# Optimization experiments

Measured on AMD Instinct MI355X. Metric: run time of the kernel, lower is better.

## Reference

```python
import jax, jax.numpy as jnp
import numpy as np

TOTAL_WORDS = 10000
EMB = 100
SEQ = 80
UNITS = 64


def setup_inputs() -> dict:
    key = jax.random.key(0)
    ks = jax.random.split(key, 10)
    B = 16384
    tokens = jax.random.randint(ks[0], (B, SEQ), 0, TOTAL_WORDS, dtype=jnp.int32)
    s = 0.05
    emb = jax.random.normal(ks[1], (TOTAL_WORDS, EMB), jnp.float32) * s
    Wx0 = jax.random.normal(ks[2], (EMB, UNITS), jnp.float32) * s
    Wh0 = jax.random.normal(ks[3], (UNITS, UNITS), jnp.float32) * s
    b0 = jnp.zeros((UNITS,), jnp.float32)
    Wx1 = jax.random.normal(ks[4], (UNITS, UNITS), jnp.float32) * s
    Wh1 = jax.random.normal(ks[5], (UNITS, UNITS), jnp.float32) * s
    b1 = jnp.zeros((UNITS,), jnp.float32)
    Wout = jax.random.normal(ks[6], (UNITS, 1), jnp.float32) * s
    bout = jnp.zeros((1,), jnp.float32)
    return {"tokens": tokens, "emb": emb, "Wx0": Wx0, "Wh0": Wh0, "b0": b0,
            "Wx1": Wx1, "Wh1": Wh1, "b1": b1, "Wout": Wout, "bout": bout}


def reference(tokens, emb, Wx0, Wh0, b0, Wx1, Wh1, b1, Wout, bout):
    # Embedding lookup: [B, SEQ, EMB]
    x = emb[tokens]
    B = tokens.shape[0]
    # time-major for scan: [SEQ, B, EMB]
    xt = jnp.transpose(x, (1, 0, 2))
    h0 = jnp.zeros((B, UNITS), x.dtype)
    h1 = jnp.zeros((B, UNITS), x.dtype)

    def step(carry, x_t):
        h0, h1 = carry
        # SimpleRNNCell (inference, dropout inactive): h' = tanh(x Wx + h Wh + b)
        h0n = jnp.tanh(x_t @ Wx0 + h0 @ Wh0 + b0)
        h1n = jnp.tanh(h0n @ Wx1 + h1 @ Wh1 + b1)
        return (h0n, h1n), None

    (h0, h1), _ = jax.lax.scan(step, (h0, h1), xt)
    logits = h1 @ Wout + bout  # [B, 1]
    return jax.nn.sigmoid(logits)
```

## Files before the change

kernel.cpp:

```cpp
#include <hip/hip_runtime.h>

#define TOTAL_WORDS 10000
#define EMB 100
#define SEQ 80
#define UNITS 64
#define BATCH 16384


typedef _Float16 f16x8 __attribute__((ext_vector_type(8)));
typedef _Float16 h2    __attribute__((ext_vector_type(2)));
typedef __fp16   fp16x2r __attribute__((ext_vector_type(2)));
typedef float    f32x4 __attribute__((ext_vector_type(4)));
typedef unsigned int u32;
typedef u32      u32x4 __attribute__((ext_vector_type(4)));

__device__ __forceinline__ u32 tanh_pk(float x, float y) {
    h2 v = __builtin_bit_cast(h2, __builtin_amdgcn_cvt_pkrtz(x, y));
    const _Float16 c3 = (_Float16)(-0.33333333f);
    const _Float16 c5 = (_Float16)(0.13333333f);
    h2 x2 = v * v;
    h2 p  = x2 * c5 + c3;
    h2 x3 = x2 * v;
    h2 r  = x3 * p + v;
    return __builtin_bit_cast(u32, r);
}

__device__ __forceinline__ f16x8 tanh_frag(f32x4 a, f32x4 b) {
    u32x4 w;
    w.x = tanh_pk(a[0], a[1]);
    w.y = tanh_pk(a[2], a[3]);
    w.z = tanh_pk(b[0], b[1]);
    w.w = tanh_pk(b[2], b[3]);
    return __builtin_bit_cast(f16x8, w);
}

__global__ void prep_kernel(const float* __restrict__ emb,
                            const float* __restrict__ Wx0,
                            const float* __restrict__ b0,
                            const float* __restrict__ Wh0,
                            const float* __restrict__ Wx1,
                            const float* __restrict__ Wh1,
                            float* __restrict__ embW,
                            _Float16* __restrict__ wfrags) {
    int b = blockIdx.x;
    if (b < 250) {
        __shared__ float wx[EMB * UNITS];
        for (int i = threadIdx.x; i < EMB * UNITS; i += 256)
            wx[i] = Wx0[i];
        __syncthreads();
        const int u = threadIdx.x & 63;
        const int wvi = threadIdx.x >> 6;
        const int vbase = b * 40 + wvi * 10;
        const float bias = b0[u];
        float acc[10];
#pragma unroll
        for (int i = 0; i < 10; ++i) acc[i] = bias;
        const float* er = emb + vbase * EMB;
#pragma unroll 4
        for (int k = 0; k < EMB; ++k) {
            float wxv = wx[k * UNITS + u];
#pragma unroll
            for (int i = 0; i < 10; ++i)
                acc[i] = fmaf(er[i * EMB + k], wxv, acc[i]);
        }
#pragma unroll
        for (int i = 0; i < 10; ++i)
            embW[(vbase + i) * UNITS + u] = acc[i];
    } else {
        int e = (b - 250) * 256 + threadIdx.x;
        int mat = e >> 12;
        int ee = e & 4095;
        int f = ee >> 9;
        int mt = f >> 1, kf = f & 1;
        int rr = ee & 511;
        int l = rr >> 3, j = rr & 7;
        int k = kf * 32 + (l >> 4) * 8 + j;
        int mm = l & 15;
        int col = 32 * (mt >> 1) + 8 * (mm >> 2) + 4 * (mt & 1) + (mm & 3);
        const float* W = (mat == 0) ? Wh0 : (mat == 1) ? Wx1 : Wh1;
        wfrags[e] = (_Float16)W[k * UNITS + col];
    }
}

#define MF(A, B, C) __builtin_amdgcn_mfma_f32_16x16x32_f16(A, B, C, 0, 0, 0)

#define RNN_ITER(EJ, TOK5)                                                    \
    {                                                                         \
                       \
        f32x4 c0 = MF(wh[0][0], h1f0, b1v[0]);                                \
        f32x4 c1 = MF(wh[1][0], h1f0, b1v[1]);                                \
        f32x4 c2 = MF(wh[2][0], h1f0, b1v[2]);                                \
        f32x4 c3 = MF(wh[3][0], h1f0, b1v[3]);                                \
                              \
        f32x4 a0 = MF(w0[0][0], h0f0, EJ[0]);                                 \
        f32x4 a1 = MF(w0[1][0], h0f0, EJ[1]);                                 \
        f32x4 a2 = MF(w0[2][0], h0f0, EJ[2]);                                 \
        f32x4 a3 = MF(w0[3][0], h0f0, EJ[3]);                                 \
                                                        \
        c0 = MF(wh[0][1], h1f1, c0);                                          \
        c1 = MF(wh[1][1], h1f1, c1);                                          \
        c2 = MF(wh[2][1], h1f1, c2);                                          \
        c3 = MF(wh[3][1], h1f1, c3);                                          \
                      \
        {                                                                     \
            const f32x4* pe = embq + (size_t)(TOK5) * 16;                     \
            EJ[0] = pe[0]; EJ[1] = pe[1]; EJ[2] = pe[8]; EJ[3] = pe[9];       \
        }                                                                     \
                                                        \
        a0 = MF(w0[0][1], h0f1, a0);                                          \
        a1 = MF(w0[1][1], h0f1, a1);                                          \
        a2 = MF(w0[2][1], h0f1, a2);                                          \
        a3 = MF(w0[3][1], h0f1, a3);                                          \
                                       \
        c0 = MF(wx[0][0], h0f0, c0);                                          \
        c1 = MF(wx[1][0], h0f0, c1);                                          \
        c2 = MF(wx[2][0], h0f0, c2);                                          \
        c3 = MF(wx[3][0], h0f0, c3);                                          \
                                  \
        f16x8 nh0f0 = tanh_frag(a0, a1);                                      \
        f16x8 nh0f1 = tanh_frag(a2, a3);                                      \
                                       \
        c0 = MF(wx[0][1], h0f1, c0);                                          \
        c1 = MF(wx[1][1], h0f1, c1);                                          \
        c2 = MF(wx[2][1], h0f1, c2);                                          \
        c3 = MF(wx[3][1], h0f1, c3);                                          \
        h0f0 = nh0f0; h0f1 = nh0f1;                                           \
        h1f0 = tanh_frag(c0, c1);                                             \
        h1f1 = tanh_frag(c2, c3);                                             \
    }

__global__ __launch_bounds__(64, 1) void rnn_mfma_kernel(
    const int*      __restrict__ tokens,
    const float*    __restrict__ embW,
    const _Float16* __restrict__ wfrags,
    const float*    __restrict__ b1,
    const float*    __restrict__ Wout,
    const float*    __restrict__ bout,
    float*          __restrict__ out) {
    const int l = threadIdx.x;
    const int q = l >> 4;
    const int n = l & 15;
    const int row0 = blockIdx.x * 16;

    const f16x8* wf8 = (const f16x8*)wfrags;
    f16x8 w0[4][2], wx[4][2], wh[4][2];
#pragma unroll
    for (int t = 0; t < 4; ++t)
#pragma unroll
        for (int kf = 0; kf < 2; ++kf) {
            w0[t][kf] = wf8[(t * 2 + kf) * 64 + l];
            wx[t][kf] = wf8[(8 + t * 2 + kf) * 64 + l];
            wh[t][kf] = wf8[(16 + t * 2 + kf) * 64 + l];
        }

    const f32x4* b1v4 = (const f32x4*)b1;
    f32x4 b1v[4];
    b1v[0] = b1v4[0 + 2 * q];
    b1v[1] = b1v4[1 + 2 * q];
    b1v[2] = b1v4[8 + 2 * q];
    b1v[3] = b1v4[9 + 2 * q];

    const f32x4* embq = (const f32x4*)embW + 2 * q;
    const int tokbase = (row0 + n) * SEQ;

    int4 tkA = *(const int4*)&tokens[tokbase];
    int4 tk  = *(const int4*)&tokens[tokbase + 4];

    f16x8 h0f0, h0f1, h1f0, h1f1;
    {
        const f32x4* pe = embq + (size_t)tkA.x * 16;
        f32x4 p0 = pe[0], p1 = pe[1], p2 = pe[8], p3 = pe[9];
        h0f0 = tanh_frag(p0, p1);
        h0f1 = tanh_frag(p2, p3);
    }
#pragma unroll
    for (int j = 0; j < 8; ++j) { h1f0[j] = (_Float16)0.0f; h1f1[j] = (_Float16)0.0f; }

    f32x4 e0[4], e1[4], e2[4], e3[4];
    {
        const f32x4* pe;
        pe = embq + (size_t)tkA.y * 16; e0[0]=pe[0]; e0[1]=pe[1]; e0[2]=pe[8]; e0[3]=pe[9];
        pe = embq + (size_t)tkA.z * 16; e1[0]=pe[0]; e1[1]=pe[1]; e1[2]=pe[8]; e1[3]=pe[9];
        pe = embq + (size_t)tkA.w * 16; e2[0]=pe[0]; e2[1]=pe[1]; e2[2]=pe[8]; e2[3]=pe[9];
        pe = embq + (size_t)tk.x  * 16; e3[0]=pe[0]; e3[1]=pe[1]; e3[2]=pe[8]; e3[3]=pe[9];
    }

    for (int k = 0; k < SEQ / 4; ++k) {
        int off = (4 * k + 8 <= SEQ - 4) ? (4 * k + 8) : (SEQ - 4);
        int4 tkC = *(const int4*)&tokens[tokbase + off];

        RNN_ITER(e0, tk.y)
        RNN_ITER(e1, tk.z)
        RNN_ITER(e2, tk.w)
        RNN_ITER(e3, tkC.x)

        tk = tkC;
    }

    {
        f32x4 wo0 = ((const f32x4*)Wout)[2 * q];
        f32x4 wo1 = ((const f32x4*)Wout)[2 * q + 1];
        f32x4 wo2 = ((const f32x4*)Wout)[8 + 2 * q];
        f32x4 wo3 = ((const f32x4*)Wout)[8 + 2 * q + 1];
        float accv = 0.0f;
#pragma unroll
        for (int j = 0; j < 4; ++j) {
            accv = fmaf((float)h1f0[j],     wo0[j], accv);
            accv = fmaf((float)h1f0[4 + j], wo1[j], accv);
            accv = fmaf((float)h1f1[j],     wo2[j], accv);
            accv = fmaf((float)h1f1[4 + j], wo3[j], accv);
        }
        accv += __shfl_down(accv, 16);
        accv += __shfl_down(accv, 32);
        if (l < 16) {
            float z = accv + bout[0];
            out[row0 + n] = 1.0f / (1.0f + __expf(-z));
        }
    }
}

extern "C" void kernel_launch(void* const* d_in, const int* in_sizes, int n_in,
                              void* d_out, int out_size, void* d_ws, size_t ws_size,
                              hipStream_t stream) {
    const int*   tokens = (const int*)d_in[0];
    const float* emb    = (const float*)d_in[1];
    const float* Wx0    = (const float*)d_in[2];
    const float* Wh0    = (const float*)d_in[3];
    const float* b0     = (const float*)d_in[4];
    const float* Wx1    = (const float*)d_in[5];
    const float* Wh1    = (const float*)d_in[6];
    const float* b1     = (const float*)d_in[7];
    const float* Wout   = (const float*)d_in[8];
    const float* bout   = (const float*)d_in[9];
    float* out = (float*)d_out;

    float* embW = (float*)d_ws;
    _Float16* wfrags =
        (_Float16*)((char*)d_ws + (size_t)TOTAL_WORDS * UNITS * 4);

    prep_kernel<<<298, 256, 0, stream>>>(emb, Wx0, b0, Wh0, Wx1, Wh1,
                                         embW, wfrags);
    rnn_mfma_kernel<<<BATCH / 16, 64, 0, stream>>>(tokens, embW, wfrags,
                                                   b1, Wout, bout, out);
}
```

Baseline: 139.1 us.

## Process two independent 16-row groups per wavefront to interleave RNN chains

Each wavefront now carries two independent batch tiles (32 rows) and interleaves their MFMA chains and tanh steps, so the latency of one dependent chain can be hidden by the other. Grid size is halved to 512 blocks. Weight fragments are pinned to AGPRs and the bias to VGPRs with empty asm constraints to relieve register pressure. The initial hidden state now starts at zero and processes token 0 through the normal step rather than a special-cased tanh of the embedding. Risks are higher register pressure and fewer blocks to fill the 256 CUs.

```diff
diff --git a/kernel.cpp b/kernel.cpp
--- a/kernel.cpp
+++ b/kernel.cpp
@@ -13,6 +13,9 @@
 typedef float    f32x4 __attribute__((ext_vector_type(4)));
 typedef unsigned int u32;
 typedef u32      u32x4 __attribute__((ext_vector_type(4)));
+
+#define PINV(x) asm volatile("" : "+v"(x))
+#define PINA(x) asm volatile("" : "+a"(x))
 
 __device__ __forceinline__ u32 tanh_pk(float x, float y) {
     h2 v = __builtin_bit_cast(h2, __builtin_amdgcn_cvt_pkrtz(x, y));
@@ -84,49 +87,79 @@
 
 #define MF(A, B, C) __builtin_amdgcn_mfma_f32_16x16x32_f16(A, B, C, 0, 0, 0)
 
-#define RNN_ITER(EJ, TOK5)                                                    \
+#define ELOAD(S, TOK)                                                         \
     {                                                                         \
-                       \
-        f32x4 c0 = MF(wh[0][0], h1f0, b1v[0]);                                \
-        f32x4 c1 = MF(wh[1][0], h1f0, b1v[1]);                                \
-        f32x4 c2 = MF(wh[2][0], h1f0, b1v[2]);                                \
-        f32x4 c3 = MF(wh[3][0], h1f0, b1v[3]);                                \
+        const f32x4* pe = embq + (size_t)(TOK) * 16;                          \
+        S[0] = pe[0]; S[1] = pe[1]; S[2] = pe[8]; S[3] = pe[9];               \
+    }
+
+#define STEP2(EG, EH, TG, TH)                                                 \
+    {                                                                         \
                               \
-        f32x4 a0 = MF(w0[0][0], h0f0, EJ[0]);                                 \
-        f32x4 a1 = MF(w0[1][0], h0f0, EJ[1]);                                 \
-        f32x4 a2 = MF(w0[2][0], h0f0, EJ[2]);                                 \
-        f32x4 a3 = MF(w0[3][0], h0f0, EJ[3]);                                 \
-                                                        \
-        c0 = MF(wh[0][1], h1f1, c0);                                          \
-        c1 = MF(wh[1][1], h1f1, c1);                                          \
-        c2 = MF(wh[2][1], h1f1, c2);                                          \
-        c3 = MF(wh[3][1], h1f1, c3);                                          \
-                      \
-        {                                                                     \
-            const f32x4* pe = embq + (size_t)(TOK5) * 16;                     \
-            EJ[0] = pe[0]; EJ[1] = pe[1]; EJ[2] = pe[8]; EJ[3] = pe[9];       \
-        }                                                                     \
-                                                        \
-        a0 = MF(w0[0][1], h0f1, a0);                                          \
-        a1 = MF(w0[1][1], h0f1, a1);                                          \
-        a2 = MF(w0[2][1], h0f1, a2);                                          \
-        a3 = MF(w0[3][1], h0f1, a3);                                          \
-                                       \
-        c0 = MF(wx[0][0], h0f0, c0);                                          \
-        c1 = MF(wx[1][0], h0f0, c1);                                          \
-        c2 = MF(wx[2][0], h0f0, c2);                                          \
-        c3 = MF(wx[3][0], h0f0, c3);                                          \
-                                  \
-        f16x8 nh0f0 = tanh_frag(a0, a1);                                      \
-        f16x8 nh0f1 = tanh_frag(a2, a3);                                      \
-                                       \
-        c0 = MF(wx[0][1], h0f1, c0);                                          \
-        c1 = MF(wx[1][1], h0f1, c1);                                          \
-        c2 = MF(wx[2][1], h0f1, c2);                                          \
-        c3 = MF(wx[3][1], h0f1, c3);                                          \
-        h0f0 = nh0f0; h0f1 = nh0f1;                                           \
-        h1f0 = tanh_frag(c0, c1);                                             \
-        h1f1 = tanh_frag(c2, c3);                                             \
+        f32x4 aG0 = MF(w0[0][0], h0G0, EG[0]);                                \
+        f32x4 aG1 = MF(w0[1][0], h0G0, EG[1]);                                \
+        f32x4 aG2 = MF(w0[2][0], h0G0, EG[2]);                                \
+        f32x4 aG3 = MF(w0[3][0], h0G0, EG[3]);                                \
+        f32x4 aH0 = MF(w0[0][0], h0H0, EH[0]);                                \
+        f32x4 aH1 = MF(w0[1][0], h0H0, EH[1]);                                \
+        f32x4 aH2 = MF(w0[2][0], h0H0, EH[2]);                                \
+        f32x4 aH3 = MF(w0[3][0], h0H0, EH[3]);                                \
+                                                             \
+        aG0 = MF(w0[0][1], h0G1, aG0);                                        \
+        aG1 = MF(w0[1][1], h0G1, aG1);                                        \
+        aG2 = MF(w0[2][1], h0G1, aG2);                                        \
+        aG3 = MF(w0[3][1], h0G1, aG3);                                        \
+        aH0 = MF(w0[0][1], h0H1, aH0);                                        \
+        aH1 = MF(w0[1][1], h0H1, aH1);                                        \
+        aH2 = MF(w0[2][1], h0H1, aH2);                                        \
+        aH3 = MF(w0[3][1], h0H1, aH3);                                        \
+                                        \
+        f32x4 cG0 = MF(wh[0][0], h1G0, b1v[0]);                               \
+        f32x4 cG1 = MF(wh[1][0], h1G0, b1v[1]);                               \
+        f32x4 cG2 = MF(wh[2][0], h1G0, b1v[2]);                               \
+        f32x4 cG3 = MF(wh[3][0], h1G0, b1v[3]);                               \
+        f32x4 cH0 = MF(wh[0][0], h1H0, b1v[0]);                               \
+        f32x4 cH1 = MF(wh[1][0], h1H0, b1v[1]);                               \
+        f32x4 cH2 = MF(wh[2][0], h1H0, b1v[2]);                               \
+        f32x4 cH3 = MF(wh[3][0], h1H0, b1v[3]);                               \
+        cG0 = MF(wh[0][1], h1G1, cG0);                                        \
+        cG1 = MF(wh[1][1], h1G1, cG1);                                        \
+        cG2 = MF(wh[2][1], h1G1, cG2);                                        \
+        cG3 = MF(wh[3][1], h1G1, cG3);                                        \
+        cH0 = MF(wh[0][1], h1H1, cH0);                                        \
+        cH1 = MF(wh[1][1], h1H1, cH1);                                        \
+        cH2 = MF(wh[2][1], h1H1, cH2);                                        \
+        cH3 = MF(wh[3][1], h1H1, cH3);                                        \
+                        \
+        ELOAD(EG, TG)                                                         \
+        ELOAD(EH, TH)                                                         \
+        \
+        h0G0 = tanh_frag(aG0, aG1);                                           \
+        h0G1 = tanh_frag(aG2, aG3);                                           \
+        h0H0 = tanh_frag(aH0, aH1);                                           \
+        h0H1 = tanh_frag(aH2, aH3);                                           \
+                                      \
+        cG0 = MF(wx[0][0], h0G0, cG0);                                        \
+        cG1 = MF(wx[1][0], h0G0, cG1);                                        \
+        cG2 = MF(wx[2][0], h0G0, cG2);                                        \
+        cG3 = MF(wx[3][0], h0G0, cG3);                                        \
+        cH0 = MF(wx[0][0], h0H0, cH0);                                        \
+        cH1 = MF(wx[1][0], h0H0, cH1);                                        \
+        cH2 = MF(wx[2][0], h0H0, cH2);                                        \
+        cH3 = MF(wx[3][0], h0H0, cH3);                                        \
+        cG0 = MF(wx[0][1], h0G1, cG0);                                        \
+        cG1 = MF(wx[1][1], h0G1, cG1);                                        \
+        cG2 = MF(wx[2][1], h0G1, cG2);                                        \
+        cG3 = MF(wx[3][1], h0G1, cG3);                                        \
+        cH0 = MF(wx[0][1], h0H1, cH0);                                        \
+        cH1 = MF(wx[1][1], h0H1, cH1);                                        \
+        cH2 = MF(wx[2][1], h0H1, cH2);                                        \
+        cH3 = MF(wx[3][1], h0H1, cH3);                                        \
+                \
+        h1G0 = tanh_frag(cG0, cG1);                                           \
+        h1G1 = tanh_frag(cG2, cG3);                                           \
+        h1H0 = tanh_frag(cH0, cH1);                                           \
+        h1H1 = tanh_frag(cH2, cH3);                                           \
     }
 
 __global__ __launch_bounds__(64, 1) void rnn_mfma_kernel(
@@ -140,7 +173,8 @@
     const int l = threadIdx.x;
     const int q = l >> 4;
     const int n = l & 15;
-    const int row0 = blockIdx.x * 16;
+    const int rowG = blockIdx.x * 32 + n;
+    const int rowH = rowG + 16;
 
     const f16x8* wf8 = (const f16x8*)wfrags;
     f16x8 w0[4][2], wx[4][2], wh[4][2];
@@ -152,6 +186,12 @@
             wx[t][kf] = wf8[(8 + t * 2 + kf) * 64 + l];
             wh[t][kf] = wf8[(16 + t * 2 + kf) * 64 + l];
         }
+#pragma unroll
+    for (int t = 0; t < 4; ++t) {
+        PINA(w0[t][0]); PINA(w0[t][1]);
+        PINA(wx[t][0]); PINA(wx[t][1]);
+        PINA(wh[t][0]); PINA(wh[t][1]);
+    }
 
     const f32x4* b1v4 = (const f32x4*)b1;
     f32x4 b1v[4];
@@ -159,42 +199,44 @@
     b1v[1] = b1v4[1 + 2 * q];
     b1v[2] = b1v4[8 + 2 * q];
     b1v[3] = b1v4[9 + 2 * q];
+    PINV(b1v[0]); PINV(b1v[1]); PINV(b1v[2]); PINV(b1v[3]);
 
     const f32x4* embq = (const f32x4*)embW + 2 * q;
-    const int tokbase = (row0 + n) * SEQ;
-
-    int4 tkA = *(const int4*)&tokens[tokbase];
-    int4 tk  = *(const int4*)&tokens[tokbase + 4];
-
-    f16x8 h0f0, h0f1, h1f0, h1f1;
-    {
-        const f32x4* pe = embq + (size_t)tkA.x * 16;
-        f32x4 p0 = pe[0], p1 = pe[1], p2 = pe[8], p3 = pe[9];
-        h0f0 = tanh_frag(p0, p1);
-        h0f1 = tanh_frag(p2, p3);
-    }
-#pragma unroll
-    for (int j = 0; j < 8; ++j) { h1f0[j] = (_Float16)0.0f; h1f1[j] = (_Float16)0.0f; }
-
-    f32x4 e0[4], e1[4], e2[4], e3[4];
-    {
-        const f32x4* pe;
-        pe = embq + (size_t)tkA.y * 16; e0[0]=pe[0]; e0[1]=pe[1]; e0[2]=pe[8]; e0[3]=pe[9];
-        pe = embq + (size_t)tkA.z * 16; e1[0]=pe[0]; e1[1]=pe[1]; e1[2]=pe[8]; e1[3]=pe[9];
-        pe = embq + (size_t)tkA.w * 16; e2[0]=pe[0]; e2[1]=pe[1]; e2[2]=pe[8]; e2[3]=pe[9];
-        pe = embq + (size_t)tk.x  * 16; e3[0]=pe[0]; e3[1]=pe[1]; e3[2]=pe[8]; e3[3]=pe[9];
-    }
+    const int tokbaseG = rowG * SEQ;
+    const int tokbaseH = rowH * SEQ;
+
+    int4 curG = *(const int4*)&tokens[tokbaseG];
+    int4 nxtG = *(const int4*)&tokens[tokbaseG + 4];
+    int4 curH = *(const int4*)&tokens[tokbaseH];
+    int4 nxtH = *(const int4*)&tokens[tokbaseH + 4];
+
+    f16x8 h0G0, h0G1, h1G0, h1G1, h0H0, h0H1, h1H0, h1H1;
+#pragma unroll
+    for (int j = 0; j < 8; ++j) {
+        h0G0[j] = (_Float16)0.0f; h0G1[j] = (_Float16)0.0f;
+        h1G0[j] = (_Float16)0.0f; h1G1[j] = (_Float16)0.0f;
+        h0H0[j] = (_Float16)0.0f; h0H1[j] = (_Float16)0.0f;
+        h1H0[j] = (_Float16)0.0f; h1H1[j] = (_Float16)0.0f;
+    }
+
+    f32x4 gA[4], gB[4], hA[4], hB[4];
+    ELOAD(gA, curG.x)
+    ELOAD(gB, curG.y)
+    ELOAD(hA, curH.x)
+    ELOAD(hB, curH.y)
 
     for (int k = 0; k < SEQ / 4; ++k) {
         int off = (4 * k + 8 <= SEQ - 4) ? (4 * k + 8) : (SEQ - 4);
-        int4 tkC = *(const int4*)&tokens[tokbase + off];
-
-        RNN_ITER(e0, tk.y)
-        RNN_ITER(e1, tk.z)
-        RNN_ITER(e2, tk.w)
-        RNN_ITER(e3, tkC.x)
-
-        tk = tkC;
+        int4 nnG = *(const int4*)&tokens[tokbaseG + off];
+        int4 nnH = *(const int4*)&tokens[tokbaseH + off];
+
+        STEP2(gA, hA, curG.z, curH.z)
+        STEP2(gB, hB, curG.w, curH.w)
+        STEP2(gA, hA, nxtG.x, nxtH.x)
+        STEP2(gB, hB, nxtG.y, nxtH.y)
+
+        curG = nxtG; nxtG = nnG;
+        curH = nxtH; nxtH = nnH;
     }
 
     {
@@ -202,19 +244,27 @@
         f32x4 wo1 = ((const f32x4*)Wout)[2 * q + 1];
         f32x4 wo2 = ((const f32x4*)Wout)[8 + 2 * q];
         f32x4 wo3 = ((const f32x4*)Wout)[8 + 2 * q + 1];
-        float accv = 0.0f;
+        float bo = bout[0];
+
+        float aG = 0.0f, aH = 0.0f;
 #pragma unroll
         for (int j = 0; j < 4; ++j) {
-            accv = fmaf((float)h1f0[j],     wo0[j], accv);
-            accv = fmaf((float)h1f0[4 + j], wo1[j], accv);
-            accv = fmaf((float)h1f1[j],     wo2[j], accv);
-            accv = fmaf((float)h1f1[4 + j], wo3[j], accv);
-        }
-        accv += __shfl_down(accv, 16);
-        accv += __shfl_down(accv, 32);
+            aG = fmaf((float)h1G0[j],     wo0[j], aG);
+            aG = fmaf((float)h1G0[4 + j], wo1[j], aG);
+            aG = fmaf((float)h1G1[j],     wo2[j], aG);
+            aG = fmaf((float)h1G1[4 + j], wo3[j], aG);
+            aH = fmaf((float)h1H0[j],     wo0[j], aH);
+            aH = fmaf((float)h1H0[4 + j], wo1[j], aH);
+            aH = fmaf((float)h1H1[j],     wo2[j], aH);
+            aH = fmaf((float)h1H1[4 + j], wo3[j], aH);
+        }
+        aG += __shfl_down(aG, 16);
+        aG += __shfl_down(aG, 32);
+        aH += __shfl_down(aH, 16);
+        aH += __shfl_down(aH, 32);
         if (l < 16) {
-            float z = accv + bout[0];
-            out[row0 + n] = 1.0f / (1.0f + __expf(-z));
+            out[rowG] = 1.0f / (1.0f + __expf(-(aG + bo)));
+            out[rowH] = 1.0f / (1.0f + __expf(-(aH + bo)));
         }
     }
 }
@@ -240,6 +290,6 @@
 
     prep_kernel<<<298, 256, 0, stream>>>(emb, Wx0, b0, Wh0, Wx1, Wh1,
                                          embW, wfrags);
-    rnn_mfma_kernel<<<BATCH / 16, 64, 0, stream>>>(tokens, embW, wfrags,
+    rnn_mfma_kernel<<<BATCH / 32, 64, 0, stream>>>(tokens, embW, wfrags,
                                                    b1, Wout, bout, out);
 }
```

Result: slower. 154.7 us (+11.2%).
